# Performance work log

Measured on AMD Instinct MI355X. Metric: run time of the kernel, lower is better.

The kernel has to match this reference:

```python
import jax, jax.numpy as jnp
import numpy as np

K = 5          # knn_step1 = DenseDilatedKnnGraph(5, 1, ...)
BN_EPS = 1e-5  # torch BatchNorm2d default


def setup_inputs() -> dict:
    key = jax.random.key(0)
    k0, k1, k2 = jax.random.split(key, 3)
    B, C, H, W = 8, 128, 256, 256
    x = jax.random.normal(k0, (B, C, H, W), dtype=jnp.float32)
    # conv_seq params: 3x3 conv (no bias), BN affine, 1x1 conv (no bias)
    w1 = jax.random.normal(k1, (C, C, 3, 3), dtype=jnp.float32) * (1.0 / np.sqrt(C * 9))
    gamma = jnp.ones((C,), dtype=jnp.float32)
    beta = jnp.zeros((C,), dtype=jnp.float32)
    w2 = jax.random.normal(k2, (C, C, 1, 1), dtype=jnp.float32) * (1.0 / np.sqrt(C))
    return {"x": x, "w1": w1, "gamma": gamma, "beta": beta, "w2": w2}


def _forward(x, w1, gamma, beta, w2):
    B, C, H, W = x.shape  # H == W required by the original module
    # x_mean[b, n] = mean_{c,w} x[b,c,n,w] + mean_{c,h} x[b,c,h,n]   (B, N)
    xm = x.mean(axis=(1, 3)) + x.mean(axis=(1, 2))
    # DenseDilatedKnnGraph: L2-normalize along channel dim (C=1 -> sign),
    # pairwise sq-distance, top-k nearest (indices built under no_grad in torch)
    v = xm * 0.5
    s = v / jnp.maximum(jnp.abs(v), 1e-12)              # F.normalize, dim=1, C=1
    dist = (s[:, :, None] - s[:, None, :]) ** 2          # (B, N, N), feature dim 1
    _, nn_idx = jax.lax.top_k(-dist, K)                  # (B, N, K) nearest neighbors
    nn_idx = jax.lax.stop_gradient(nn_idx)
    # batched_index_select: gather node features at neighbor indices
    gathered = jax.vmap(lambda f, i: f[i])(xm, nn_idx)   # (B, N, K)
    gate = jax.nn.sigmoid(gathered.sum(axis=-1))         # (B, N)
    # x3.transpose(1,2) * x + x  ->  broadcast gate over channels and width
    y = gate[:, None, :, None] * x + x                   # (B, C, H, W)
    dn = ("NCHW", "OIHW", "NCHW")
    h = jax.lax.conv_general_dilated(y, w1, (1, 1), "SAME", dimension_numbers=dn)
    # BatchNorm2d, training-mode batch statistics (biased variance)
    mu = h.mean(axis=(0, 2, 3), keepdims=True)
    var = h.var(axis=(0, 2, 3), keepdims=True)
    h = (h - mu) * jax.lax.rsqrt(var + BN_EPS)
    h = h * gamma[None, :, None, None] + beta[None, :, None, None]
    h = jax.nn.relu(h)
    out = jax.lax.conv_general_dilated(h, w2, (1, 1), "SAME", dimension_numbers=dn)
    return out


def reference(x, w1, gamma, beta, w2):
    return _forward(x, w1, gamma, beta, w2)
```

## Files before the change

### kernel.cpp

```cpp
#include <hip/hip_runtime.h>
#include <hip/hip_bf16.h>
#include <math.h>

constexpr int B = 8, C = 128, H = 256, W = 256, NN = 256, KNN = 5;
constexpr int HW = H * W;

constexpr int WS_ROWSUM = 0;
constexpr int WS_COLSUM = 2048;
constexpr int WS_GMUL   = 4096;
constexpr int WS_SCALE  = 6144;
constexpr int WS_BIAS   = 6272;
constexpr int WS_PART   = 8192;
constexpr int WS_WT     = 24576;
constexpr int WS_W2T    = 98304;
constexpr size_t WS_Y_BYTES_OFF = 512 * 1024;
constexpr size_t Y_BYTES = (size_t)B * H * W * C * 2;

typedef __attribute__((ext_vector_type(8))) short bf16x8;
typedef __attribute__((ext_vector_type(4))) float f32x4;

union U4 { uint4 q; bf16x8 v; unsigned short u[8]; };

__device__ inline unsigned short f2bf(float f) {
    __hip_bfloat16 h = __float2bfloat16(f);
    return *reinterpret_cast<unsigned short*>(&h);
}
__device__ inline float bf2f(unsigned short u) {
    __hip_bfloat16 h = *reinterpret_cast<__hip_bfloat16*>(&u);
    return __bfloat162float(h);
}

__global__ __launch_bounds__(256) void k_sums(const float* __restrict__ x,
                                              float* __restrict__ ws) {
    const int b = blockIdx.x >> 7;
    const int c = blockIdx.x & 127;
    const int t = threadIdx.x;
    const int wv = t >> 6;
    const float4* p4 = (const float4*)(x + (size_t)(b * C + c) * HW);
    __shared__ float srow[256];
    __shared__ float scol[4][256];
    float ca0 = 0.f, ca1 = 0.f, ca2 = 0.f, ca3 = 0.f;
    for (int it = 0; it < 64; ++it) {
        const float4 v = p4[it * 256 + t];
        ca0 += v.x; ca1 += v.y; ca2 += v.z; ca3 += v.w;
        float s = v.x + v.y + v.z + v.w;
#pragma unroll
        for (int m = 1; m < 64; m <<= 1) s += __shfl_xor(s, m);
        if ((t & 63) == 0) srow[it * 4 + wv] = s;
    }
    const int cb = (t & 63) * 4;
    scol[wv][cb + 0] = ca0;
    scol[wv][cb + 1] = ca1;
    scol[wv][cb + 2] = ca2;
    scol[wv][cb + 3] = ca3;
    __syncthreads();
    atomicAdd(&ws[WS_ROWSUM + b * 256 + t], srow[t]);
    atomicAdd(&ws[WS_COLSUM + b * 256 + t],
              scol[0][t] + scol[1][t] + scol[2][t] + scol[3][t]);
}

__global__ void k_gate(float* __restrict__ ws) {
    const int b = blockIdx.x;
    const int i = threadIdx.x;
    __shared__ float xm[256], sgn[256];
    const float v = ws[WS_ROWSUM + b * 256 + i] * (1.f / 32768.f)
                  + ws[WS_COLSUM + b * 256 + i] * (1.f / 32768.f);
    xm[i] = v;
    const float vv = v * 0.5f;
    sgn[i] = vv / fmaxf(fabsf(vv), 1e-12f);
    __syncthreads();
    const float si = sgn[i];
    float bd[KNN];
    int bi[KNN];
    for (int k = 0; k < KNN; ++k) { bd[k] = 1e30f; bi[k] = 0; }
    for (int j = 0; j < NN; ++j) {
        float d = si - sgn[j];
        d *= d;
        if (d < bd[KNN - 1]) {
            int p = KNN - 1;
            while (p > 0 && bd[p - 1] > d) {
                bd[p] = bd[p - 1];
                bi[p] = bi[p - 1];
                --p;
            }
            bd[p] = d;
            bi[p] = j;
        }
    }
    float gs = 0.f;
    for (int k = 0; k < KNN; ++k) gs += xm[bi[k]];
    const float gate = 1.f / (1.f + expf(-gs));
    ws[WS_GMUL + b * 256 + i] = 1.f + gate;
}

__global__ __launch_bounds__(256) void k_ygenT(const float* __restrict__ x,
                                               const float* __restrict__ ws,
                                               unsigned short* __restrict__ y) {
    const int b = blockIdx.x >> 8;
    const int h = blockIdx.x & 255;
    const int w = threadIdx.x;
    const float g = ws[WS_GMUL + b * 256 + h];
    const float* xp = x + ((size_t)(b * C) * H + h) * W + w;
    unsigned short* yp = y + (((size_t)(b * H) + h) * 16) * (W * 8);
    for (int c8 = 0; c8 < 16; ++c8) {
        U4 pk;
#pragma unroll
        for (int j = 0; j < 8; ++j)
            pk.u[j] = f2bf(xp[(size_t)(c8 * 8 + j) * HW] * g);
        *reinterpret_cast<uint4*>(yp + ((size_t)c8 * W + w) * 8) = pk.q;
    }
}

__global__ void k_wprep(const float* __restrict__ w1, unsigned short* __restrict__ wt) {
    const int e = blockIdx.x * 256 + threadIdx.x;
    const int j = e & 7;
    const int kg = (e >> 3) & 3;
    const int och = (e >> 5) & 127;
    const int s = e >> 12;
    const int c = (s & 3) * 32 + kg * 8 + j;
    const int pos = s >> 2;
    const int ky = pos / 3, kx = pos - ky * 3;
    wt[e] = f2bf(w1[(((size_t)och * C + c) * 3 + ky) * 3 + kx]);
}

__global__ void k_wprep2(const float* __restrict__ w2, unsigned short* __restrict__ w2t) {
    const int e = blockIdx.x * 256 + threadIdx.x;
    const int kk = e & 31;
    const int och = (e >> 5) & 127;
    const int s = e >> 12;
    const int k = s * 32 + kk;
    const int c = k >> 2;
    const int t4 = k & 3;
    const float w = w2[och * C + c];
    const unsigned short hi = f2bf(w);
    w2t[e] = (t4 < 2) ? hi : f2bf(w - bf2f(hi));
}

__global__ __launch_bounds__(256) void k_conv3d(const unsigned short* __restrict__ y2,
                                                const unsigned short* __restrict__ wt,
                                                float* __restrict__ ws,
                                                float* __restrict__ hout) {
    const int bx0 = blockIdx.x;
    const int bx = (bx0 & 7) * 512 + (bx0 >> 3);
    const int whalf = bx & 1;
    const int hrow = (bx >> 1) & 255;
    const int b = bx >> 9;
    const int w0 = whalf * 128;

    const int t = threadIdx.x;
    const int wv = t >> 6;
    const int l = t & 63;
    const int wm = wv >> 1, wn = wv & 1;
    const int lr = l & 15, lq = l >> 4;

    __shared__ float sPart[4][128][2];

    f32x4 acc[4][4];
#pragma unroll
    for (int i = 0; i < 4; ++i)
#pragma unroll
        for (int j = 0; j < 4; ++j) acc[i][j] = (f32x4){0.f, 0.f, 0.f, 0.f};

    const unsigned short* aptr = wt + (size_t)(wm * 64 + lr) * 32 + lq * 8;
    const int scb = w0 + wn * 64 + lr - 1;

    uint4 pa[4], pb[4];

    auto loadA = [&](int s, uint4* d) {
        const unsigned short* p = aptr + (size_t)s * 4096;
#pragma unroll
        for (int mf = 0; mf < 4; ++mf)
            d[mf] = *reinterpret_cast<const uint4*>(p + mf * 512);
    };
    auto loadB = [&](int s, uint4* d) {
        const int pos = s >> 2;
        const int ky = pos / 3, kx = pos - ky * 3;
        const int sr = hrow + ky - 1;
        const bool rok = (unsigned)sr < (unsigned)H;
        const int c8 = (s & 3) * 4 + lq;
        const unsigned short* rb =
            y2 + (((size_t)(b * 256 + (rok ? sr : 0)) * 16 + c8) * 256) * 8;
#pragma unroll
        for (int nf = 0; nf < 4; ++nf) {
            const int sc = scb + nf * 16 + kx;
            const bool ok = rok && ((unsigned)sc < (unsigned)W);
            const uint4 q = *reinterpret_cast<const uint4*>(rb + (size_t)(ok ? sc : 0) * 8);
            const uint4 z = {0u, 0u, 0u, 0u};
            d[nf] = ok ? q : z;
        }
    };

    loadA(0, pa);
    loadB(0, pb);
    for (int s = 0; s < 36; ++s) {
        uint4 ca[4], cb[4];
#pragma unroll
        for (int i = 0; i < 4; ++i) { ca[i] = pa[i]; cb[i] = pb[i]; }
        if (s + 1 < 36) {
            loadA(s + 1, pa);
            loadB(s + 1, pb);
        }
#pragma unroll
        for (int mf = 0; mf < 4; ++mf) {
            U4 am; am.q = ca[mf];
#pragma unroll
            for (int nf = 0; nf < 4; ++nf) {
                U4 bm; bm.q = cb[nf];
                acc[mf][nf] = __builtin_amdgcn_mfma_f32_16x16x32_bf16(
                    am.v, bm.v, acc[mf][nf], 0, 0, 0);
            }
        }
    }

#pragma unroll
    for (int mf = 0; mf < 4; ++mf) {
#pragma unroll
        for (int reg = 0; reg < 4; ++reg) {
            const int och = wm * 64 + mf * 16 + lq * 4 + reg;
            float* orow = hout + (((size_t)(b * C + och) * H + hrow) * W) + w0;
#pragma unroll
            for (int nf = 0; nf < 4; ++nf)
                orow[wn * 64 + nf * 16 + lr] = acc[mf][nf][reg];
        }
    }

#pragma unroll
    for (int mf = 0; mf < 4; ++mf) {
#pragma unroll
        for (int reg = 0; reg < 4; ++reg) {
            float s = 0.f, q = 0.f;
#pragma unroll
            for (int nf = 0; nf < 4; ++nf) {
                const float v = acc[mf][nf][reg];
                s += v;
                q = fmaf(v, v, q);
            }
#pragma unroll
            for (int m = 1; m < 16; m <<= 1) {
                s += __shfl_xor(s, m);
                q += __shfl_xor(q, m);
            }
            if (lr == 0) {
                const int och = wm * 64 + mf * 16 + lq * 4 + reg;
                sPart[wv][och][0] = s;
                sPart[wv][och][1] = q;
            }
        }
    }
    __syncthreads();
    {
        const int o = t & 127;
        const int which = t >> 7;
        const int wmn = o >> 6;
        const float v = sPart[wmn * 2][o][which] + sPart[wmn * 2 + 1][o][which];
        atomicAdd(&ws[WS_PART + o * 128 + (bx & 63) * 2 + which], v);
    }
}

__device__ inline bf16x8 b_fetch(const float* __restrict__ x, int b, int s,
                                 int hrow, int w0, int px, int kg,
                                 float g0, float g1, float g2) {
    const int pos = s >> 2;
    const int ky = pos / 3, kx = pos - ky * 3;
    const int cbase = (s & 3) * 32 + kg * 8;
    int crow = hrow + ky - 1;
    int col = w0 + px + kx - 1;
    const float g = (ky == 0) ? g0 : ((ky == 1) ? g1 : g2);
    const float sc = ((unsigned)col < (unsigned)W) ? g : 0.f;
    crow = min(max(crow, 0), H - 1);
    col = min(max(col, 0), W - 1);
    const float* p = x + (((size_t)(b * C + cbase) * H + crow) * W + col);
    union { bf16x8 v8; unsigned short u[8]; } r;
#pragma unroll
    for (int j = 0; j < 8; ++j) r.u[j] = f2bf(p[(size_t)j * HW] * sc);
    return r.v8;
}

__global__ __launch_bounds__(256) void k_conv3(const float* __restrict__ x,
                                               const unsigned short* __restrict__ wt,
                                               float* __restrict__ ws,
                                               float* __restrict__ hout) {
    const int bx = blockIdx.x;
    const int whalf = bx & 1;
    const int hrow = (bx >> 1) & 255;
    const int b = bx >> 9;
    const int w0 = whalf * 128;

    const int t = threadIdx.x;
    const int wv = t >> 6;
    const int l = t & 63;
    const int wm = wv >> 1, wn = wv & 1;
    const int lr = l & 15, lq = l >> 4;

    __shared__ unsigned short sA[128 * 40];
    __shared__ unsigned short sB[128 * 40];
    __shared__ float sPart[4][128][2];

    float g0, g1, g2;
    {
        const int r0 = hrow - 1, r2 = hrow + 1;
        g0 = (r0 >= 0) ? ws[WS_GMUL + b * 256 + r0] : 0.f;
        g1 = ws[WS_GMUL + b * 256 + hrow];
        g2 = (r2 < H) ? ws[WS_GMUL + b * 256 + r2] : 0.f;
    }

    f32x4 acc[4][4];
#pragma unroll
    for (int i = 0; i < 4; ++i)
#pragma unroll
        for (int j = 0; j < 4; ++j) acc[i][j] = (f32x4){0.f, 0.f, 0.f, 0.f};

    const int a_och = t & 127, a_h = t >> 7;
    const int b_px = t & 127, b_kg0 = t >> 7;
    const int b_kg1 = b_kg0 + 2;

    uint4 pa0, pa1;
    bf16x8 pb0, pb1;
    {
        const uint4* asrc = reinterpret_cast<const uint4*>(wt + (size_t)a_och * 32 + a_h * 16);
        pa0 = asrc[0];
        pa1 = asrc[1];
        pb0 = b_fetch(x, b, 0, hrow, w0, b_px, b_kg0, g0, g1, g2);
        pb1 = b_fetch(x, b, 0, hrow, w0, b_px, b_kg1, g0, g1, g2);
    }

    for (int s = 0; s < 36; ++s) {
        __syncthreads();
        *reinterpret_cast<uint4*>(&sA[a_och * 40 + a_h * 16]) = pa0;
        *reinterpret_cast<uint4*>(&sA[a_och * 40 + a_h * 16 + 8]) = pa1;
        *reinterpret_cast<bf16x8*>(&sB[b_px * 40 + b_kg0 * 8]) = pb0;
        *reinterpret_cast<bf16x8*>(&sB[b_px * 40 + b_kg1 * 8]) = pb1;
        __syncthreads();

        if (s + 1 < 36) {
            const uint4* asrc = reinterpret_cast<const uint4*>(
                wt + (size_t)(s + 1) * 4096 + (size_t)a_och * 32 + a_h * 16);
            pa0 = asrc[0];
            pa1 = asrc[1];
            pb0 = b_fetch(x, b, s + 1, hrow, w0, b_px, b_kg0, g0, g1, g2);
            pb1 = b_fetch(x, b, s + 1, hrow, w0, b_px, b_kg1, g0, g1, g2);
        }

        bf16x8 af[4], bfr[4];
#pragma unroll
        for (int mf = 0; mf < 4; ++mf) {
            const int och = wm * 64 + mf * 16 + lr;
            af[mf] = *reinterpret_cast<const bf16x8*>(&sA[och * 40 + lq * 8]);
        }
#pragma unroll
        for (int nf = 0; nf < 4; ++nf) {
            const int px = wn * 64 + nf * 16 + lr;
            bfr[nf] = *reinterpret_cast<const bf16x8*>(&sB[px * 40 + lq * 8]);
        }
#pragma unroll
        for (int mf = 0; mf < 4; ++mf)
#pragma unroll
            for (int nf = 0; nf < 4; ++nf)
                acc[mf][nf] = __builtin_amdgcn_mfma_f32_16x16x32_bf16(
                    af[mf], bfr[nf], acc[mf][nf], 0, 0, 0);
    }

#pragma unroll
    for (int mf = 0; mf < 4; ++mf) {
#pragma unroll
        for (int reg = 0; reg < 4; ++reg) {
            const int och = wm * 64 + mf * 16 + lq * 4 + reg;
            float* orow = hout + (((size_t)(b * C + och) * H + hrow) * W) + w0;
#pragma unroll
            for (int nf = 0; nf < 4; ++nf)
                orow[wn * 64 + nf * 16 + lr] = acc[mf][nf][reg];
        }
    }

#pragma unroll
    for (int mf = 0; mf < 4; ++mf) {
#pragma unroll
        for (int reg = 0; reg < 4; ++reg) {
            float s = 0.f, q = 0.f;
#pragma unroll
            for (int nf = 0; nf < 4; ++nf) {
                const float v = acc[mf][nf][reg];
                s += v;
                q = fmaf(v, v, q);
            }
#pragma unroll
            for (int m = 1; m < 16; m <<= 1) {
                s += __shfl_xor(s, m);
                q += __shfl_xor(q, m);
            }
            if (lr == 0) {
                const int och = wm * 64 + mf * 16 + lq * 4 + reg;
                sPart[wv][och][0] = s;
                sPart[wv][och][1] = q;
            }
        }
    }
    __syncthreads();
    {
        const int o = t & 127;
        const int which = t >> 7;
        const int wmn = o >> 6;
        const float v = sPart[wmn * 2][o][which] + sPart[wmn * 2 + 1][o][which];
        atomicAdd(&ws[WS_PART + o * 128 + (bx & 63) * 2 + which], v);
    }
}

__global__ void k_scalebias(const float* __restrict__ gamma,
                            const float* __restrict__ beta, float* __restrict__ ws) {
    const int c = threadIdx.x;
    const float* p = ws + WS_PART + c * 128;
    float s = 0.f, q = 0.f;
    for (int i = 0; i < 64; ++i) {
        s += p[i * 2];
        q += p[i * 2 + 1];
    }
    const float cnt = (float)B * HW;
    const float mu = s / cnt;
    const float var = q / cnt - mu * mu;
    const float rs = rsqrtf(var + 1e-5f);
    const float sc = rs * gamma[c];
    ws[WS_SCALE + c] = sc;
    ws[WS_BIAS + c] = beta[c] - mu * sc;
}

__global__ __launch_bounds__(256) void k_conv1d(float* __restrict__ io,
                                                const unsigned short* __restrict__ w2t,
                                                const float* __restrict__ ws) {
    const int bx = blockIdx.x;
    const int pblk = bx & 511;
    const int b = bx >> 9;
    const size_t p0 = (size_t)pblk * 128;

    const int t = threadIdx.x;
    const int wv = t >> 6;
    const int l = t & 63;
    const int wm = wv >> 1, wn = wv & 1;
    const int lr = l & 15, lq = l >> 4;

    __shared__ float sSB[128][2];
    if (t < 128) {
        sSB[t][0] = ws[WS_SCALE + t];
        sSB[t][1] = ws[WS_BIAS + t];
    }
    __syncthreads();

    f32x4 acc[4][4];
#pragma unroll
    for (int i = 0; i < 4; ++i)
#pragma unroll
        for (int j = 0; j < 4; ++j) acc[i][j] = (f32x4){0.f, 0.f, 0.f, 0.f};

    const unsigned short* aptr = w2t + (size_t)(wm * 64 + lr) * 32 + lq * 8;
    const float* hb = io + (size_t)b * C * HW + p0 + wn * 64 + lr;

    uint4 pa[4], pb[4];

    auto loadA = [&](int s, uint4* d) {
        const unsigned short* p = aptr + (size_t)s * 4096;
#pragma unroll
        for (int mf = 0; mf < 4; ++mf)
            d[mf] = *reinterpret_cast<const uint4*>(p + mf * 512);
    };
    auto loadB = [&](int s, uint4* d) {
        const int c0 = s * 8 + lq * 2;
        const float s0 = sSB[c0][0], o0 = sSB[c0][1];
        const float s1 = sSB[c0 + 1][0], o1 = sSB[c0 + 1][1];
        const float* pp0 = hb + (size_t)c0 * HW;
        const float* pp1 = hb + (size_t)(c0 + 1) * HW;
#pragma unroll
        for (int nf = 0; nf < 4; ++nf) {
            const float v0 = fmaxf(fmaf(pp0[nf * 16], s0, o0), 0.f);
            const float v1 = fmaxf(fmaf(pp1[nf * 16], s1, o1), 0.f);
            const unsigned short hi0 = f2bf(v0);
            const unsigned short lo0 = f2bf(v0 - bf2f(hi0));
            const unsigned short hi1 = f2bf(v1);
            const unsigned short lo1 = f2bf(v1 - bf2f(hi1));
            U4 fr;
            fr.u[0] = hi0; fr.u[1] = lo0; fr.u[2] = hi0; fr.u[3] = lo0;
            fr.u[4] = hi1; fr.u[5] = lo1; fr.u[6] = hi1; fr.u[7] = lo1;
            d[nf] = fr.q;
        }
    };

    loadA(0, pa);
    loadB(0, pb);
    for (int s = 0; s < 16; ++s) {
        uint4 ca[4], cb[4];
#pragma unroll
        for (int i = 0; i < 4; ++i) { ca[i] = pa[i]; cb[i] = pb[i]; }
        if (s + 1 < 16) {
            loadA(s + 1, pa);
            loadB(s + 1, pb);
        }
#pragma unroll
        for (int mf = 0; mf < 4; ++mf) {
            U4 am; am.q = ca[mf];
#pragma unroll
            for (int nf = 0; nf < 4; ++nf) {
                U4 bm; bm.q = cb[nf];
                acc[mf][nf] = __builtin_amdgcn_mfma_f32_16x16x32_bf16(
                    am.v, bm.v, acc[mf][nf], 0, 0, 0);
            }
        }
    }

    __syncthreads();

#pragma unroll
    for (int mf = 0; mf < 4; ++mf) {
#pragma unroll
        for (int reg = 0; reg < 4; ++reg) {
            const int och = wm * 64 + mf * 16 + lq * 4 + reg;
            float* orow = io + (size_t)(b * C + och) * HW + p0;
#pragma unroll
            for (int nf = 0; nf < 4; ++nf)
                orow[wn * 64 + nf * 16 + lr] = acc[mf][nf][reg];
        }
    }
}

extern "C" void kernel_launch(void* const* d_in, const int* in_sizes, int n_in,
                              void* d_out, int out_size, void* d_ws, size_t ws_size,
                              hipStream_t stream) {
    const float* x = (const float*)d_in[0];
    const float* w1 = (const float*)d_in[1];
    const float* gamma = (const float*)d_in[2];
    const float* beta = (const float*)d_in[3];
    const float* w2 = (const float*)d_in[4];
    float* out = (float*)d_out;
    float* ws = (float*)d_ws;
    unsigned short* wt = (unsigned short*)(ws + WS_WT);
    unsigned short* w2t = (unsigned short*)(ws + WS_W2T);

    hipMemsetAsync(d_ws, 0, 98304, stream);
    k_wprep<<<576, 256, 0, stream>>>(w1, wt);
    k_wprep2<<<256, 256, 0, stream>>>(w2, w2t);
    k_sums<<<B * C, 256, 0, stream>>>(x, ws);
    k_gate<<<B, 256, 0, stream>>>(ws);

    if (ws_size >= WS_Y_BYTES_OFF + Y_BYTES) {
        unsigned short* y2 = (unsigned short*)((char*)d_ws + WS_Y_BYTES_OFF);
        k_ygenT<<<B * H, 256, 0, stream>>>(x, ws, y2);
        k_conv3d<<<B * 256 * 2, 256, 0, stream>>>(y2, wt, ws, out);
    } else {
        k_conv3<<<B * 256 * 2, 256, 0, stream>>>(x, wt, ws, out);
    }

    k_scalebias<<<1, 128, 0, stream>>>(gamma, beta, ws);
    k_conv1d<<<B * 512, 256, 0, stream>>>(out, w2t, ws);
}
```

Measured before the change: 607.5 us.

## Pad bf16 activation buffer with zero halo to remove conv boundary checks

The intermediate bf16 activation buffer gets a one-pixel zero border in H and W (258x258), filled by a new small zeroing kernel. The 3x3 conv's B-operand loads no longer need per-element bounds checks or selects and use 32-bit unsigned offsets instead of 64-bit pointer math. The 1x1 conv also switches to 32-bit offset indexing. In exchange the buffer grows slightly, there is an extra kernel launch, and the offsets must stay within 32-bit range.

```diff
diff --git a/kernel.cpp b/kernel.cpp
--- a/kernel.cpp
+++ b/kernel.cpp
@@ -14,7 +14,11 @@
 constexpr int WS_WT     = 24576;
 constexpr int WS_W2T    = 98304;
 constexpr size_t WS_Y_BYTES_OFF = 512 * 1024;
-constexpr size_t Y_BYTES = (size_t)B * H * W * C * 2;
+
+constexpr int Y2P_CS = 258 * 8;
+constexpr int Y2P_HS = 16 * Y2P_CS;
+constexpr int Y2P_BS = 258 * Y2P_HS;
+constexpr size_t Y2P_BYTES = (size_t)B * Y2P_BS * 2;
 
 typedef __attribute__((ext_vector_type(8))) short bf16x8;
 typedef __attribute__((ext_vector_type(4))) float f32x4;
@@ -93,6 +97,28 @@
     ws[WS_GMUL + b * 256 + i] = 1.f + gate;
 }
 
+__global__ __launch_bounds__(256) void k_yzero(unsigned short* __restrict__ y) {
+    const int id = blockIdx.x * 256 + threadIdx.x;
+    const uint4 z = {0u, 0u, 0u, 0u};
+    if (id < 66048) {
+        const int per = Y2P_HS / 8;
+        const int b = id / (2 * per);
+        const int r = id % (2 * per);
+        const int hp = (r >= per) ? 257 : 0;
+        const int off = (r >= per) ? r - per : r;
+        *reinterpret_cast<uint4*>(y + (size_t)b * Y2P_BS + (size_t)hp * Y2P_HS + off * 8) = z;
+    } else {
+        const int id2 = id - 66048;
+        const int b = id2 >> 13;
+        const int r = id2 & 8191;
+        const int hp = (r >> 5) + 1;
+        const int c8 = (r >> 1) & 15;
+        const int wp = (r & 1) ? 257 : 0;
+        *reinterpret_cast<uint4*>(y + (size_t)b * Y2P_BS + (size_t)hp * Y2P_HS
+                                  + c8 * Y2P_CS + wp * 8) = z;
+    }
+}
+
 __global__ __launch_bounds__(256) void k_ygenT(const float* __restrict__ x,
                                                const float* __restrict__ ws,
                                                unsigned short* __restrict__ y) {
@@ -101,13 +127,13 @@
     const int w = threadIdx.x;
     const float g = ws[WS_GMUL + b * 256 + h];
     const float* xp = x + ((size_t)(b * C) * H + h) * W + w;
-    unsigned short* yp = y + (((size_t)(b * H) + h) * 16) * (W * 8);
+    unsigned short* yp = y + (size_t)b * Y2P_BS + (size_t)(h + 1) * Y2P_HS + (w + 1) * 8;
     for (int c8 = 0; c8 < 16; ++c8) {
         U4 pk;
 #pragma unroll
         for (int j = 0; j < 8; ++j)
             pk.u[j] = f2bf(xp[(size_t)(c8 * 8 + j) * HW] * g);
-        *reinterpret_cast<uint4*>(yp + ((size_t)c8 * W + w) * 8) = pk.q;
+        *reinterpret_cast<uint4*>(yp + c8 * Y2P_CS) = pk.q;
     }
 }
 
@@ -161,33 +187,27 @@
 #pragma unroll
         for (int j = 0; j < 4; ++j) acc[i][j] = (f32x4){0.f, 0.f, 0.f, 0.f};
 
-    const unsigned short* aptr = wt + (size_t)(wm * 64 + lr) * 32 + lq * 8;
-    const int scb = w0 + wn * 64 + lr - 1;
+    const unsigned aoff = (unsigned)((wm * 64 + lr) * 32 + lq * 8);
+    const unsigned laneB = (unsigned)(lq * Y2P_CS + (w0 + wn * 64 + lr) * 8);
+    const unsigned bbase = (unsigned)(b * Y2P_BS);
 
     uint4 pa[4], pb[4];
 
     auto loadA = [&](int s, uint4* d) {
-        const unsigned short* p = aptr + (size_t)s * 4096;
+        const unsigned so = aoff + (unsigned)(s * 4096);
 #pragma unroll
         for (int mf = 0; mf < 4; ++mf)
-            d[mf] = *reinterpret_cast<const uint4*>(p + mf * 512);
+            d[mf] = *reinterpret_cast<const uint4*>(wt + so + mf * 512);
     };
     auto loadB = [&](int s, uint4* d) {
         const int pos = s >> 2;
         const int ky = pos / 3, kx = pos - ky * 3;
-        const int sr = hrow + ky - 1;
-        const bool rok = (unsigned)sr < (unsigned)H;
-        const int c8 = (s & 3) * 4 + lq;
-        const unsigned short* rb =
-            y2 + (((size_t)(b * 256 + (rok ? sr : 0)) * 16 + c8) * 256) * 8;
-#pragma unroll
-        for (int nf = 0; nf < 4; ++nf) {
-            const int sc = scb + nf * 16 + kx;
-            const bool ok = rok && ((unsigned)sc < (unsigned)W);
-            const uint4 q = *reinterpret_cast<const uint4*>(rb + (size_t)(ok ? sc : 0) * 8);
-            const uint4 z = {0u, 0u, 0u, 0u};
-            d[nf] = ok ? q : z;
-        }
+        const int cc = s & 3;
+        const unsigned sbase = bbase + (unsigned)((hrow + ky) * Y2P_HS + cc * 4 * Y2P_CS)
+                             + laneB + (unsigned)(kx * 8);
+#pragma unroll
+        for (int nf = 0; nf < 4; ++nf)
+            d[nf] = *reinterpret_cast<const uint4*>(y2 + sbase + nf * 128);
     };
 
     loadA(0, pa);
@@ -450,27 +470,27 @@
 #pragma unroll
         for (int j = 0; j < 4; ++j) acc[i][j] = (f32x4){0.f, 0.f, 0.f, 0.f};
 
-    const unsigned short* aptr = w2t + (size_t)(wm * 64 + lr) * 32 + lq * 8;
-    const float* hb = io + (size_t)b * C * HW + p0 + wn * 64 + lr;
+    const unsigned aoff = (unsigned)((wm * 64 + lr) * 32 + lq * 8);
+    const float* hplane = io + (size_t)b * C * HW;
+    const unsigned vbase = (unsigned)(p0 + wn * 64 + lr);
 
     uint4 pa[4], pb[4];
 
     auto loadA = [&](int s, uint4* d) {
-        const unsigned short* p = aptr + (size_t)s * 4096;
+        const unsigned so = aoff + (unsigned)(s * 4096);
 #pragma unroll
         for (int mf = 0; mf < 4; ++mf)
-            d[mf] = *reinterpret_cast<const uint4*>(p + mf * 512);
+            d[mf] = *reinterpret_cast<const uint4*>(w2t + so + mf * 512);
     };
     auto loadB = [&](int s, uint4* d) {
         const int c0 = s * 8 + lq * 2;
         const float s0 = sSB[c0][0], o0 = sSB[c0][1];
         const float s1 = sSB[c0 + 1][0], o1 = sSB[c0 + 1][1];
-        const float* pp0 = hb + (size_t)c0 * HW;
-        const float* pp1 = hb + (size_t)(c0 + 1) * HW;
+        const unsigned off0 = (unsigned)c0 * (unsigned)HW + vbase;
 #pragma unroll
         for (int nf = 0; nf < 4; ++nf) {
-            const float v0 = fmaxf(fmaf(pp0[nf * 16], s0, o0), 0.f);
-            const float v1 = fmaxf(fmaf(pp1[nf * 16], s1, o1), 0.f);
+            const float v0 = fmaxf(fmaf(hplane[off0 + nf * 16], s0, o0), 0.f);
+            const float v1 = fmaxf(fmaf(hplane[off0 + HW + nf * 16], s1, o1), 0.f);
             const unsigned short hi0 = f2bf(v0);
             const unsigned short lo0 = f2bf(v0 - bf2f(hi0));
             const unsigned short hi1 = f2bf(v1);
@@ -538,8 +558,9 @@
     k_sums<<<B * C, 256, 0, stream>>>(x, ws);
     k_gate<<<B, 256, 0, stream>>>(ws);
 
-    if (ws_size >= WS_Y_BYTES_OFF + Y_BYTES) {
+    if (ws_size >= WS_Y_BYTES_OFF + Y2P_BYTES) {
         unsigned short* y2 = (unsigned short*)((char*)d_ws + WS_Y_BYTES_OFF);
+        k_yzero<<<514, 256, 0, stream>>>(y2);
         k_ygenT<<<B * H, 256, 0, stream>>>(x, ws, y2);
         k_conv3d<<<B * 256 * 2, 256, 0, stream>>>(y2, wt, ws, out);
     } else {
```

Measured after the change: 612.6 us. Within noise of the previous version (+0.8%).
